# Optimization experiments

Hardware: AMD Instinct MI355X
Metric: run time of the kernel (lower is better)

Reference implementation:

```python
import jax, jax.numpy as jnp
import numpy as np

N, K, H, W = 2048, 8, 128, 128
G = 50              # glimpse size (50x50 from tem_rnn input 50*50)
ENC = 100           # glimpse encoder output (relation_rnn input arithmetic)
HID = 256
D_REL = ENC + (3 + 50) * 2 + HID          # 462
D_TEM = G * G + (3 + 50) * 2 + HID        # 2862


def _lin(k, out_d, in_d, scale=0.02):
    k1, k2 = jax.random.split(k)
    return (jax.random.normal(k1, (out_d, in_d), jnp.float32) * scale,
            jax.random.normal(k2, (out_d,), jnp.float32) * scale)


def _lstm_params(k, in_d, hid):
    k1, k2, k3, k4 = jax.random.split(k, 4)
    s = 0.02
    return (jax.random.normal(k1, (4 * hid, in_d), jnp.float32) * s,
            jax.random.normal(k2, (4 * hid, hid), jnp.float32) * s,
            jax.random.normal(k3, (4 * hid,), jnp.float32) * s,
            jax.random.normal(k4, (4 * hid,), jnp.float32) * s)


def lstm_cell(x, h, c, Wih, Whh, bih, bhh):
    g = x @ Wih.T + h @ Whh.T + (bih + bhh)
    i, f, gg, o = jnp.split(g, 4, axis=-1)
    i, f, o = jax.nn.sigmoid(i), jax.nn.sigmoid(f), jax.nn.sigmoid(o)
    c2 = f * c + i * jnp.tanh(gg)
    return o * jnp.tanh(c2), c2


def _bilinear_one(im, py, px):
    # im [H,W]; py,px [G,G] pixel coords; zeros padding like torch grid_sample
    x0 = jnp.floor(px); y0 = jnp.floor(py)
    wx1 = px - x0; wy1 = py - y0
    x0i = x0.astype(jnp.int32); y0i = y0.astype(jnp.int32)

    def gather(yi, xi):
        valid = (yi >= 0) & (yi < H) & (xi >= 0) & (xi < W)
        v = im[jnp.clip(yi, 0, H - 1), jnp.clip(xi, 0, W - 1)]
        return jnp.where(valid, v, 0.0)

    return ((1 - wy1) * (1 - wx1) * gather(y0i, x0i)
            + (1 - wy1) * wx1 * gather(y0i, x0i + 1)
            + wy1 * (1 - wx1) * gather(y0i + 1, x0i)
            + wy1 * wx1 * gather(y0i + 1, x0i + 1))


def stn_glimpse(z_where, img):
    # z_where [n,3] = (scale, tx, ty); theta = [[s,0,tx],[0,s,ty]] (attentive_stn_encode)
    s, tx, ty = z_where[:, 0], z_where[:, 1], z_where[:, 2]
    lin = jnp.linspace(-1.0, 1.0, G)
    gy, gx = jnp.meshgrid(lin, lin, indexing='ij')           # [G,G]
    px = (s[:, None, None] * gx + tx[:, None, None] + 1.0) * 0.5 * (W - 1)
    py = (s[:, None, None] * gy + ty[:, None, None] + 1.0) * 0.5 * (H - 1)
    out = jax.vmap(_bilinear_one)(img, py, px)               # [n,G,G]
    return out.reshape(out.shape[0], G * G)


def setup_inputs() -> dict:
    key = jax.random.key(0)
    ks = jax.random.split(key, 16)
    inp = {
        'img': jax.random.uniform(ks[0], (N, H, W), jnp.float32),
        'z_what_last': jax.random.normal(ks[1], (N, K, 50), jnp.float32),
        'z_where_last': jax.random.normal(ks[2], (N, K, 3), jnp.float32) * 0.3,
        'z_pres_last': jnp.ones((N, K, 1), jnp.float32),
        'hidden_last': jax.random.normal(ks[3], (N, K, HID), jnp.float32),
    }
    inp['W_loca'], inp['b_loca'] = _lin(ks[4], 3, HID)
    inp['Wg'], inp['bg'] = _lin(ks[5], ENC, G * G)
    (inp['Wih_rel'], inp['Whh_rel'], inp['bih_rel'], inp['bhh_rel']) = _lstm_params(ks[6], D_REL, HID)
    (inp['Wih_tem'], inp['Whh_tem'], inp['bih_tem'], inp['bhh_tem']) = _lstm_params(ks[7], D_TEM, HID)
    inp['Wm_wh'], inp['bm_wh'] = _lin(ks[8], 3, HID + 3)
    inp['Ws_wh'], inp['bs_wh'] = _lin(ks[9], 3, HID + 3)
    inp['Wm_wt'], inp['bm_wt'] = _lin(ks[10], 50, 50 + HID + HID)
    inp['Ws_wt'], inp['bs_wt'] = _lin(ks[11], 50, 50 + HID + HID)
    inp['Wm_pr'], inp['bm_pr'] = _lin(ks[12], 1, 50 + 3 + HID + HID)
    inp['Ws_pr'], inp['bs_pr'] = _lin(ks[13], 1, 50 + 3 + HID + HID)
    return inp


def reference(img, z_what_last, z_where_last, z_pres_last, hidden_last,
              W_loca, b_loca, Wg, bg,
              Wih_rel, Whh_rel, bih_rel, bhh_rel,
              Wih_tem, Whh_tem, bih_tem, bhh_tem,
              Wm_wh, bm_wh, Ws_wh, bs_wh,
              Wm_wt, bm_wt, Ws_wt, bs_wt,
              Wm_pr, bm_pr, Ws_pr, bs_pr):
    n = img.shape[0]

    def step(carry, xs):
        h_r, c_r, pzw, pzwhat = carry
        zwl, zwhatl, zpl, hl = xs   # [n,3],[n,50],[n,1],[n,256]
        # prop_loca: relu(linear(hidden)) + z_where_last
        zwb = jax.nn.relu(hl @ W_loca.T + b_loca) + zwl
        # STN glimpse + encode (bias pass)
        enc = jax.nn.relu(stn_glimpse(zwb, img) @ Wg.T + bg)        # [n,100]
        rin = jnp.concatenate([enc, zwl, pzw, zwhatl, pzwhat, hl], -1)  # [n,462]
        h_r2, c_r2 = lstm_cell(rin, h_r, c_r, Wih_rel, Whh_rel, bih_rel, bhh_rel)
        # z_where: latent predictor mean (eval mode)
        zw = jnp.concatenate([zwl, h_r2], -1) @ Wm_wh.T + bm_wh      # [n,3]
        # second STN glimpse with sampled where
        g2 = stn_glimpse(zw, img)                                    # [n,2500]
        tin = jnp.concatenate([g2, zw, pzw, zwhatl, pzwhat, hl], -1) # [n,2862]
        h_t, c_t = lstm_cell(tin, h_r2, c_r2, Wih_tem, Whh_tem, bih_tem, bhh_tem)
        # z_what mean
        zwhat = jnp.concatenate([zwhatl, h_r2, h_t], -1) @ Wm_wt.T + bm_wt  # [n,50]
        # z_pres: deterministic expectation of Bernoulli(mean*std) * previous pres
        zp_cal = jnp.concatenate([zwhat, zw, h_r2, h_t], -1)
        p = jax.nn.sigmoid(zp_cal @ Wm_pr.T + bm_pr) * jax.nn.sigmoid(zp_cal @ Ws_pr.T + bs_pr)
        zp = p * zpl                                                 # [n,1]
        return (h_r2, c_r2, zw, zwhat), (zwhat, zw, zp, h_t)

    carry0 = (jnp.zeros((n, HID), img.dtype), jnp.zeros((n, HID), img.dtype),
              jnp.zeros((n, 3), img.dtype), jnp.zeros((n, 50), img.dtype))
    xs = (jnp.swapaxes(z_where_last, 0, 1), jnp.swapaxes(z_what_last, 0, 1),
          jnp.swapaxes(z_pres_last, 0, 1), jnp.swapaxes(hidden_last, 0, 1))
    _, (zwhat_s, zw_s, zp_s, ht_s) = jax.lax.scan(step, carry0, xs)
    z_what = jnp.swapaxes(zwhat_s, 0, 1)   # [n,K,50]
    z_where = jnp.swapaxes(zw_s, 0, 1)     # [n,K,3]
    z_pres = jnp.swapaxes(zp_s, 0, 1)      # [n,K,1]
    h_temp = jnp.swapaxes(ht_s, 0, 1)      # [n,K,256]
    return z_what, z_where, z_pres, h_temp
```

## Files before the change

kernel.cpp:

```cpp
#include <hip/hip_runtime.h>
#include <hip/hip_bf16.h>
#include <math.h>

typedef __attribute__((ext_vector_type(8))) short bf16x8;
typedef __attribute__((ext_vector_type(4))) float f32x4;
using bf16 = __hip_bfloat16;

constexpr int NN   = 2048;
constexpr int KO   = 8;
constexpr int IH   = 128, IW = 128;
constexpr int GS   = 50;
constexpr int GG2  = GS*GS;
constexpr int HIDD = 256;
constexpr int RIN_LD = 768;
constexpr int TIN_LD = 3136;
constexpr int G1_LD  = 2560;

__device__ __forceinline__ float sigm(float x) { return 1.f/(1.f+expf(-x)); }

template<int OUT_BF16, int RELU>
__global__ __launch_bounds__(256, 2) void mfma_gemm(
    const bf16* __restrict__ A, int lda, int Kd,
    const bf16* __restrict__ Wt, int ldw, int M,
    const float* __restrict__ b1, const float* __restrict__ b2,
    void* __restrict__ Cout, int ldc)
{
    __shared__ bf16x8 As16[512];
    __shared__ bf16x8 Bs16[512];
    const int tid  = threadIdx.x;
    const int n0   = blockIdx.y*64;
    const int m0   = blockIdx.x*64;
    const int wave = tid>>6, lane = tid&63;
    const int wy   = wave>>1, wx = wave&1;

    const int row = tid>>2, part = tid&3;
    const bf16* Ap = A + (size_t)(n0+row)*lda + part*8;
    const int   wm = m0 + row;
    const bool  wok = wm < M;
    const bf16* Wp = Wt + (size_t)(wok ? wm : 0)*ldw + part*8;
    const int dst0 = ((row>>4)*2+0)*64 + part*16 + (row&15);
    const int dst1 = dst0 + 64;

    f32x4 acc[2][2] = {};
    const bf16x8 z8 = {};
    bf16x8 pa0 = *(const bf16x8*)Ap;
    bf16x8 pa1 = *(const bf16x8*)(Ap + 32);
    bf16x8 pw0 = *(const bf16x8*)Wp;
    bf16x8 pw1 = *(const bf16x8*)(Wp + 32);

    for (int k0 = 0; k0 < Kd; k0 += 64) {
        __syncthreads();
        As16[dst0] = pa0;
        As16[dst1] = pa1;
        Bs16[dst0] = wok ? pw0 : z8;
        Bs16[dst1] = wok ? pw1 : z8;
        __syncthreads();
        if (k0 + 64 < Kd) {
            pa0 = *(const bf16x8*)(Ap + k0 + 64);
            pa1 = *(const bf16x8*)(Ap + k0 + 96);
            pw0 = *(const bf16x8*)(Wp + k0 + 64);
            pw1 = *(const bf16x8*)(Wp + k0 + 96);
        }
        bf16x8 av[2][2], bv[2][2];
        #pragma unroll
        for (int i=0;i<2;i++)
            #pragma unroll
            for (int h=0;h<2;h++) av[i][h] = As16[((wy*2+i)*2+h)*64 + lane];
        #pragma unroll
        for (int j=0;j<2;j++)
            #pragma unroll
            for (int h=0;h<2;h++) bv[j][h] = Bs16[((wx*2+j)*2+h)*64 + lane];
        #pragma unroll
        for (int h=0;h<2;h++)
            #pragma unroll
            for (int i=0;i<2;i++)
                #pragma unroll
                for (int j=0;j<2;j++)
                    acc[i][j] = __builtin_amdgcn_mfma_f32_16x16x32_bf16(av[i][h], bv[j][h], acc[i][j], 0, 0, 0);
    }

    const int q = lane>>4, r = lane&15;
    #pragma unroll
    for (int j=0;j<2;j++) {
        int col = m0 + wx*32 + j*16 + r;
        if (col < M) {
            float bias = 0.f;
            if (b1) bias += b1[col];
            if (b2) bias += b2[col];
            #pragma unroll
            for (int i=0;i<2;i++) {
                #pragma unroll
                for (int reg=0;reg<4;reg++) {
                    float v = acc[i][j][reg] + bias;
                    if (RELU) v = fmaxf(v, 0.f);
                    size_t idx = (size_t)(n0 + wy*32 + i*16 + q*4 + reg)*ldc + col;
                    if (OUT_BF16) ((bf16*)Cout)[idx] = __float2bfloat16(v);
                    else          ((float*)Cout)[idx] = v;
                }
            }
        }
    }
}

__device__ __forceinline__ void glimpse_points(const float* __restrict__ im,
                                               float s, float tx, float ty,
                                               bf16* __restrict__ drow) {
    const float GXS = 2.0f/49.0f;
    const float txp = tx + 1.0f, typ = ty + 1.0f;
    for (int p2 = threadIdx.x; p2 < 1250; p2 += 256) {
        int i = p2 / 25;
        int j = (p2 - i*25) * 2;
        float gy  = fmaf((float)i, GXS, -1.0f);
        float py  = fmaf(s, gy, typ) * 63.5f;
        float y0f = floorf(py); float fy = py - y0f; int y0 = (int)y0f;
        float wy0 = ((unsigned)y0     < 128u) ? (1.f - fy) : 0.f;
        float wy1 = ((unsigned)(y0+1) < 128u) ? fy         : 0.f;
        const float* r0 = im + min(max(y0,  0),127)*IW;
        const float* r1 = im + min(max(y0+1,0),127)*IW;
        float gxa = fmaf((float)j, GXS, -1.0f);
        float pxa = fmaf(s, gxa, txp) * 63.5f;
        float xa0f = floorf(pxa); float fa = pxa - xa0f; int xa0 = (int)xa0f;
        float wa0 = ((unsigned)xa0     < 128u) ? (1.f - fa) : 0.f;
        float wa1 = ((unsigned)(xa0+1) < 128u) ? fa         : 0.f;
        int xa0c = min(max(xa0,  0),127), xa1c = min(max(xa0+1,0),127);
        float gxb = fmaf((float)(j+1), GXS, -1.0f);
        float pxb = fmaf(s, gxb, txp) * 63.5f;
        float xb0f = floorf(pxb); float fb = pxb - xb0f; int xb0 = (int)xb0f;
        float wb0 = ((unsigned)xb0     < 128u) ? (1.f - fb) : 0.f;
        float wb1 = ((unsigned)(xb0+1) < 128u) ? fb         : 0.f;
        int xb0c = min(max(xb0,  0),127), xb1c = min(max(xb0+1,0),127);

        float va = fmaf(wy1, fmaf(wa0, r1[xa0c], wa1*r1[xa1c]),
                   wy0 *     fmaf(wa0, r0[xa0c], wa1*r0[xa1c]));
        float vb = fmaf(wy1, fmaf(wb0, r1[xb0c], wb1*r1[xb1c]),
                   wy0 *     fmaf(wb0, r0[xb0c], wb1*r0[xb1c]));

        bf16 b0 = __float2bfloat16(va), b1 = __float2bfloat16(vb);
        unsigned short u0, u1;
        __builtin_memcpy(&u0, &b0, 2); __builtin_memcpy(&u1, &b1, 2);
        *(unsigned int*)(drow + i*GS + j) = (unsigned)u0 | ((unsigned)u1 << 16);
    }
}

__global__ __launch_bounds__(256) void glimpse_batch(const float* __restrict__ img,
                                                     const float* __restrict__ z,
                                                     bf16* __restrict__ dst, int ldd) {
    int b = blockIdx.x;
    const float* im = img + (size_t)(b & (NN-1))*IH*IW;
    glimpse_points(im, z[b*3+0], z[b*3+1], z[b*3+2], dst + (size_t)b*ldd);
}

__global__ __launch_bounds__(256) void glimpse2_fused(const float* __restrict__ img,
                                                      const float* __restrict__ zw_cur,
                                                      const float* __restrict__ zw_prev,
                                                      const float* __restrict__ zwhat_prev,
                                                      const float* __restrict__ z_what_last,
                                                      const float* __restrict__ hidden_last,
                                                      bf16* __restrict__ tin, int k) {
    int n = blockIdx.x;
    const float* im = img + (size_t)n*IH*IW;
    float s  = zw_cur[n*3+0];
    float tx = zw_cur[n*3+1];
    float ty = zw_cur[n*3+2];
    bf16* trow = tin + (size_t)n*TIN_LD;
    glimpse_points(im, s, tx, ty, trow);
    for (int c = threadIdx.x; c < 362; c += 256) {
        float v;
        if      (c <   3) v = (c==0) ? s : ((c==1) ? tx : ty);
        else if (c <   6) v = zw_prev[n*3 + c-3];
        else if (c <  56) v = z_what_last[((size_t)n*KO + k)*50 + c-6];
        else if (c < 106) v = zwhat_prev[n*50 + c-56];
        else              v = hidden_last[((size_t)n*KO + k)*HIDD + c-106];
        trow[2500 + c] = __float2bfloat16(v);
    }
}

__global__ void zero_f32(float* __restrict__ p, int n) {
    int i = blockIdx.x*blockDim.x + threadIdx.x;
    if (i < n) p[i] = 0.f;
}

__global__ void repack_w(const float* __restrict__ s1, int K1,
                         const float* __restrict__ s2, int K2,
                         bf16* __restrict__ dst, int ldd, int M) {
    int gid = blockIdx.x*blockDim.x + threadIdx.x;
    if (gid >= M*ldd) return;
    int m = gid / ldd, c = gid - m*ldd;
    float v = 0.f;
    if (c < K1)           v = s1[(size_t)m*K1 + c];
    else if (c < K1+K2)   v = s2[(size_t)m*K2 + (c-K1)];
    dst[gid] = __float2bfloat16(v);
}

__global__ void zwb_all_kernel(const float* __restrict__ hidden_last,
                               const float* __restrict__ z_where_last,
                               const float* __restrict__ Wl, const float* __restrict__ bl,
                               float* __restrict__ zwb_all) {
    int gid = blockIdx.x*blockDim.x + threadIdx.x;
    if (gid >= KO*NN*3) return;
    int j = gid % 3; int rn = gid/3; int n = rn & (NN-1); int s = rn >> 11;
    const float* hl = hidden_last + ((size_t)n*KO + s)*HIDD;
    const float* w  = Wl + j*HIDD;
    float acc = bl[j];
    for (int i=0;i<HIDD;i++) acc = fmaf(hl[i], w[i], acc);
    zwb_all[gid] = fmaxf(acc, 0.f) + z_where_last[((size_t)n*KO + s)*3 + j];
}

__global__ void fill_rin_static(bf16* __restrict__ rin,
                                const float* __restrict__ z_where_last,
                                const float* __restrict__ z_what_last,
                                const float* __restrict__ hidden_last,
                                int base, int CH) {
    int gid = blockIdx.x*blockDim.x + threadIdx.x;
    if (gid >= CH*NN*309) return;
    int c = gid % 309; int rn = gid/309; int n = rn & (NN-1); int sl = rn >> 11;
    int k = base + sl;
    float v; int col;
    if (c < 3)       { col = 100 + c;      v = z_where_last[((size_t)n*KO + k)*3 + c]; }
    else if (c < 53) { col = 106 + (c-3);  v = z_what_last[((size_t)n*KO + k)*50 + (c-3)]; }
    else             { col = 206 + (c-53); v = hidden_last[((size_t)n*KO + k)*HIDD + (c-53)]; }
    rin[(size_t)rn*RIN_LD + col] = __float2bfloat16(v);
}

__global__ void zero_rin_carry(bf16* __restrict__ rin0) {
    int gid = blockIdx.x*blockDim.x + threadIdx.x;
    if (gid >= NN*309) return;
    int c = gid % 309, n = gid/309;
    int col = (c < 3) ? 103+c : ((c < 53) ? 156+(c-3) : 462+(c-53));
    rin0[(size_t)n*RIN_LD + col] = __float2bfloat16(0.f);
}

__global__ __launch_bounds__(256) void rel_fused(
    const float* __restrict__ gates, float* __restrict__ h_r, float* __restrict__ c_r,
    const float* __restrict__ z_where_last,
    const float* __restrict__ Wm_wh, const float* __restrict__ bm_wh,
    float* __restrict__ zw_cur, float* __restrict__ out_zwhere,
    bf16* __restrict__ rin_next, bf16* __restrict__ tin, int k)
{
    __shared__ float hs[256];
    int n = blockIdx.x, j = threadIdx.x;
    const float* g = gates + (size_t)n*1024;
    float ig = sigm(g[j]);
    float fg = sigm(g[256+j]);
    float gg = tanhf(g[512+j]);
    float og = sigm(g[768+j]);
    int cidx = n*256 + j;
    float c2 = fg*c_r[cidx] + ig*gg;
    float hv = og*tanhf(c2);
    c_r[cidx] = c2;
    h_r[cidx] = hv;
    hs[j] = hv;
    bf16 hb = __float2bfloat16(hv);
    rin_next[(size_t)n*RIN_LD + 462 + j] = hb;
    tin[(size_t)n*TIN_LD + 2862 + j]     = hb;
    __syncthreads();
    int w = j >> 6, lane = j & 63;
    if (w < 3) {
        const float* wt = Wm_wh + w*259;
        float s = 0.f;
        for (int i = lane; i < 256; i += 64) s = fmaf(hs[i], wt[3+i], s);
        #pragma unroll
        for (int off = 32; off; off >>= 1) s += __shfl_down(s, off);
        if (lane == 0) {
            const float* zwl = z_where_last + ((size_t)n*KO + k)*3;
            float acc = bm_wh[w] + s;
            for (int i = 0; i < 3; i++) acc = fmaf(zwl[i], wt[i], acc);
            zw_cur[n*3+w] = acc;
            out_zwhere[((size_t)n*KO + k)*3 + w] = acc;
            rin_next[(size_t)n*RIN_LD + 103 + w] = __float2bfloat16(acc);
        }
    }
}

__global__ __launch_bounds__(256) void tem_fused(
    const float* __restrict__ gates, const float* __restrict__ c_r, const float* __restrict__ h_r,
    const float* __restrict__ z_what_last,
    const float* __restrict__ Wm_wt, const float* __restrict__ bm_wt,
    const float* __restrict__ Wm_pr, const float* __restrict__ bm_pr,
    const float* __restrict__ Ws_pr, const float* __restrict__ bs_pr,
    const float* __restrict__ zw_cur, const float* __restrict__ z_pres_last,
    float* __restrict__ zwhat_cur, float* __restrict__ out_zwhat,
    float* __restrict__ out_htemp, float* __restrict__ out_zpres,
    bf16* __restrict__ rin_next, int k)
{
    __shared__ float L[615];
    int n = blockIdx.x, j = threadIdx.x;
    const float* g = gates + (size_t)n*1024;
    float ig = sigm(g[j]);
    float fg = sigm(g[256+j]);
    float gg = tanhf(g[512+j]);
    float og = sigm(g[768+j]);
    float c2 = fg*c_r[n*256+j] + ig*gg;
    float hv = og*tanhf(c2);
    out_htemp[((size_t)n*KO + k)*HIDD + j] = hv;
    L[309+j] = hv;
    L[53+j]  = h_r[n*256+j];
    if (j < 50)      L[j]  = z_what_last[((size_t)n*KO + k)*50 + j];
    else if (j < 53) L[j]  = zw_cur[n*3 + (j-50)];
    __syncthreads();
    if (j < 200) {
        int m = j >> 2, part = j & 3;
        const float* wt = Wm_wt + m*562;
        float s = 0.f;
        for (int i = part; i < 562; i += 4) {
            float v = (i < 50) ? L[i] : L[i+3];
            s = fmaf(v, wt[i], s);
        }
        s += __shfl_down(s, 2);
        s += __shfl_down(s, 1);
        if (part == 0) {
            float acc = s + bm_wt[m];
            zwhat_cur[n*50+m] = acc;
            out_zwhat[((size_t)n*KO + k)*50 + m] = acc;
            rin_next[(size_t)n*RIN_LD + 156 + m] = __float2bfloat16(acc);
            L[565+m] = acc;
        }
    }
    __syncthreads();
    if (j < 64) {
        float s1 = 0.f, s2 = 0.f;
        for (int i = j; i < 565; i += 64) {
            float v = (i < 50) ? L[565+i] : L[i];
            s1 = fmaf(v, Wm_pr[i], s1);
            s2 = fmaf(v, Ws_pr[i], s2);
        }
        #pragma unroll
        for (int off = 32; off; off >>= 1) { s1 += __shfl_down(s1,off); s2 += __shfl_down(s2,off); }
        if (j == 0) {
            float p = sigm(s1 + bm_pr[0]) * sigm(s2 + bs_pr[0]);
            out_zpres[(size_t)n*KO + k] = p * z_pres_last[(size_t)n*KO + k];
        }
    }
}

extern "C" void kernel_launch(void* const* d_in, const int* in_sizes, int n_in,
                              void* d_out, int out_size, void* d_ws, size_t ws_size,
                              hipStream_t stream) {
    (void)in_sizes; (void)n_in; (void)out_size;
    const float* img          = (const float*)d_in[0];
    const float* z_what_last  = (const float*)d_in[1];
    const float* z_where_last = (const float*)d_in[2];
    const float* z_pres_last  = (const float*)d_in[3];
    const float* hidden_last  = (const float*)d_in[4];
    const float* W_loca = (const float*)d_in[5];
    const float* b_loca = (const float*)d_in[6];
    const float* Wg     = (const float*)d_in[7];
    const float* bg     = (const float*)d_in[8];
    const float* Wih_rel = (const float*)d_in[9];
    const float* Whh_rel = (const float*)d_in[10];
    const float* bih_rel = (const float*)d_in[11];
    const float* bhh_rel = (const float*)d_in[12];
    const float* Wih_tem = (const float*)d_in[13];
    const float* Whh_tem = (const float*)d_in[14];
    const float* bih_tem = (const float*)d_in[15];
    const float* bhh_tem = (const float*)d_in[16];
    const float* Wm_wh = (const float*)d_in[17];
    const float* bm_wh = (const float*)d_in[18];
    const float* Wm_wt = (const float*)d_in[21];
    const float* bm_wt = (const float*)d_in[22];
    const float* Wm_pr = (const float*)d_in[25];
    const float* bm_pr = (const float*)d_in[26];
    const float* Ws_pr = (const float*)d_in[27];
    const float* bs_pr = (const float*)d_in[28];

    char* base_p = (char*)d_ws;
    size_t off = 0;
    auto carve = [&](size_t bytes) -> char* {
        char* r = base_p + off;
        off += (bytes + 255) & ~(size_t)255;
        return r;
    };
    bf16*  tin      = (bf16*) carve((size_t)NN*TIN_LD*2);
    float* gates    = (float*)carve((size_t)NN*1024*4);
    bf16*  W_tem    = (bf16*) carve((size_t)1024*TIN_LD*2);
    bf16*  W_rel    = (bf16*) carve((size_t)1024*RIN_LD*2);
    bf16*  Wg_bf    = (bf16*) carve((size_t)100*G1_LD*2);
    float* zwb_all  = (float*)carve((size_t)KO*NN*3*4);
    float* h_r      = (float*)carve((size_t)NN*HIDD*4);
    float* c_r      = (float*)carve((size_t)NN*HIDD*4);
    float* zw1      = (float*)carve((size_t)NN*3*4);
    float* zwhat1   = (float*)carve((size_t)NN*50*4);
    float* zw0      = (float*)carve((size_t)NN*3*4);
    float* zwhat0   = (float*)carve((size_t)NN*50*4);
    size_t fixed_bytes = off;

    int CH = 1;
    for (int cand : {8, 4, 2}) {
        size_t need = fixed_bytes
                    + (((size_t)cand*NN*G1_LD*2 + 255) & ~(size_t)255)
                    + (((size_t)cand*NN*RIN_LD*2 + 255) & ~(size_t)255);
        if (need <= ws_size) { CH = cand; break; }
    }
    bf16* g1 = nullptr; int g1ld;
    bf16* rin;
    if (CH > 1) {
        g1   = (bf16*)carve((size_t)CH*NN*G1_LD*2);
        rin  = (bf16*)carve((size_t)CH*NN*RIN_LD*2);
        g1ld = G1_LD;
    } else {
        rin  = (bf16*)carve((size_t)NN*RIN_LD*2);
        g1   = tin;
        g1ld = TIN_LD;
    }

    float* out        = (float*)d_out;
    float* out_zwhat  = out;
    float* out_zwhere = out + (size_t)NN*KO*50;
    float* out_zpres  = out_zwhere + (size_t)NN*KO*3;
    float* out_htemp  = out_zpres + (size_t)NN*KO;

    {
        int nz = NN*(HIDD + 3 + 50);
        zero_f32<<<(nz+255)/256, 256, 0, stream>>>(c_r, nz);
    }
    zero_rin_carry<<<(NN*309+255)/256, 256, 0, stream>>>(rin);
    repack_w<<<((1024*RIN_LD)+255)/256, 256, 0, stream>>>(Wih_rel, 462, Whh_rel, 256, W_rel, RIN_LD, 1024);
    repack_w<<<((1024*TIN_LD)+255)/256, 256, 0, stream>>>(Wih_tem, 2862, Whh_tem, 256, W_tem, TIN_LD, 1024);
    repack_w<<<((100*G1_LD)+255)/256, 256, 0, stream>>>(Wg, 2500, nullptr, 0, Wg_bf, G1_LD, 100);
    zwb_all_kernel<<<(KO*NN*3+255)/256, 256, 0, stream>>>(hidden_last, z_where_last, W_loca, b_loca, zwb_all);

    for (int cbase = 0; cbase < KO; cbase += CH) {
        fill_rin_static<<<(CH*NN*309+255)/256, 256, 0, stream>>>(rin, z_where_last, z_what_last, hidden_last, cbase, CH);
        glimpse_batch<<<CH*NN, 256, 0, stream>>>(img, zwb_all + (size_t)cbase*NN*3, g1, g1ld);
        mfma_gemm<1,1><<<dim3(2, CH*32), 256, 0, stream>>>(g1, g1ld, G1_LD, Wg_bf, G1_LD, 100, bg, nullptr, rin, RIN_LD);

        for (int s = 0; s < CH; ++s) {
            int k = cbase + s;
            bf16* rin_k  = rin + (size_t)s*NN*RIN_LD;
            bf16* rin_nx = rin + (size_t)((s+1)%CH)*NN*RIN_LD;
            float* zw_cur     = (k & 1) ? zw1 : zw0;
            float* zw_prev    = (k & 1) ? zw0 : zw1;
            float* zwhat_cur  = (k & 1) ? zwhat1 : zwhat0;
            float* zwhat_prev = (k & 1) ? zwhat0 : zwhat1;

            mfma_gemm<0,0><<<dim3(16, 32), 256, 0, stream>>>(rin_k, RIN_LD, RIN_LD, W_rel, RIN_LD, 1024, bih_rel, bhh_rel, gates, 1024);
            rel_fused<<<NN, 256, 0, stream>>>(gates, h_r, c_r, z_where_last, Wm_wh, bm_wh, zw_cur, out_zwhere, rin_nx, tin, k);
            glimpse2_fused<<<NN, 256, 0, stream>>>(img, zw_cur, zw_prev, zwhat_prev, z_what_last, hidden_last, tin, k);
            mfma_gemm<0,0><<<dim3(16, 32), 256, 0, stream>>>(tin, TIN_LD, TIN_LD, W_tem, TIN_LD, 1024, bih_tem, bhh_tem, gates, 1024);
            tem_fused<<<NN, 256, 0, stream>>>(gates, c_r, h_r, z_what_last, Wm_wt, bm_wt, Wm_pr, bm_pr, Ws_pr, bs_pr,
                                              zw_cur, z_pres_last, zwhat_cur, out_zwhat, out_htemp, out_zpres, rin_nx, k);
        }
    }
}
```

Baseline: 1.348 ms.

## Remap GEMM blocks per XCD, stage glimpse rows in LDS, warp-reduce zwb

The GEMM launch becomes 1D, and block indices are remapped so that blocks sharing an A row-tile land on the same XCD, which should improve L2 reuse across the chiplets. The first-stage glimpse kernel copies only the image rows covered by the glimpse into shared memory (up to 64 rows) and does the bilinear gathers from LDS. It falls back to global reads when the glimpse spans more rows. The zwb projection now uses one wavefront per row with vector loads and a shuffle reduction instead of a serial per-output loop. The risks are the extra LDS footprint, which lowers occupancy for the glimpse kernel, and an added __syncthreads.

```diff
diff --git a/kernel.cpp b/kernel.cpp
--- a/kernel.cpp
+++ b/kernel.cpp
@@ -10,11 +10,11 @@
 constexpr int KO   = 8;
 constexpr int IH   = 128, IW = 128;
 constexpr int GS   = 50;
-constexpr int GG2  = GS*GS;
 constexpr int HIDD = 256;
 constexpr int RIN_LD = 768;
 constexpr int TIN_LD = 3136;
 constexpr int G1_LD  = 2560;
+constexpr int GROWS  = 64;
 
 __device__ __forceinline__ float sigm(float x) { return 1.f/(1.f+expf(-x)); }
 
@@ -23,13 +23,16 @@
     const bf16* __restrict__ A, int lda, int Kd,
     const bf16* __restrict__ Wt, int ldw, int M,
     const float* __restrict__ b1, const float* __restrict__ b2,
-    void* __restrict__ Cout, int ldc)
+    void* __restrict__ Cout, int ldc, int nxb)
 {
     __shared__ bf16x8 As16[512];
     __shared__ bf16x8 Bs16[512];
+    const int b    = blockIdx.x;
+    const int xcd  = b & 7;
+    const int t    = b >> 3;
+    const int n0   = (xcd + 8*(t / nxb))*64;
+    const int m0   = (t % nxb)*64;
     const int tid  = threadIdx.x;
-    const int n0   = blockIdx.y*64;
-    const int m0   = blockIdx.x*64;
     const int wave = tid>>6, lane = tid&63;
     const int wy   = wave>>1, wx = wave&1;
 
@@ -102,29 +105,28 @@
     }
 }
 
-__device__ __forceinline__ void glimpse_points(const float* __restrict__ im,
-                                               float s, float tx, float ty,
-                                               bf16* __restrict__ drow) {
+__device__ __forceinline__ void glimpse_points_global(const float* __restrict__ im,
+                                                      float s, float tx, float ty,
+                                                      bf16* __restrict__ drow) {
     const float GXS = 2.0f/49.0f;
     const float txp = tx + 1.0f, typ = ty + 1.0f;
     for (int p2 = threadIdx.x; p2 < 1250; p2 += 256) {
-        int i = p2 / 25;
-        int j = (p2 - i*25) * 2;
+        int i = p2 / 25, j = (p2 - i*25)*2;
         float gy  = fmaf((float)i, GXS, -1.0f);
-        float py  = fmaf(s, gy, typ) * 63.5f;
+        float py  = fmaf(s, gy, typ)*63.5f;
         float y0f = floorf(py); float fy = py - y0f; int y0 = (int)y0f;
         float wy0 = ((unsigned)y0     < 128u) ? (1.f - fy) : 0.f;
         float wy1 = ((unsigned)(y0+1) < 128u) ? fy         : 0.f;
         const float* r0 = im + min(max(y0,  0),127)*IW;
         const float* r1 = im + min(max(y0+1,0),127)*IW;
         float gxa = fmaf((float)j, GXS, -1.0f);
-        float pxa = fmaf(s, gxa, txp) * 63.5f;
+        float pxa = fmaf(s, gxa, txp)*63.5f;
         float xa0f = floorf(pxa); float fa = pxa - xa0f; int xa0 = (int)xa0f;
         float wa0 = ((unsigned)xa0     < 128u) ? (1.f - fa) : 0.f;
         float wa1 = ((unsigned)(xa0+1) < 128u) ? fa         : 0.f;
         int xa0c = min(max(xa0,  0),127), xa1c = min(max(xa0+1,0),127);
         float gxb = fmaf((float)(j+1), GXS, -1.0f);
-        float pxb = fmaf(s, gxb, txp) * 63.5f;
+        float pxb = fmaf(s, gxb, txp)*63.5f;
         float xb0f = floorf(pxb); float fb = pxb - xb0f; int xb0 = (int)xb0f;
         float wb0 = ((unsigned)xb0     < 128u) ? (1.f - fb) : 0.f;
         float wb1 = ((unsigned)(xb0+1) < 128u) ? fb         : 0.f;
@@ -145,9 +147,63 @@
 __global__ __launch_bounds__(256) void glimpse_batch(const float* __restrict__ img,
                                                      const float* __restrict__ z,
                                                      bf16* __restrict__ dst, int ldd) {
+    __shared__ float rows[GROWS*IW];
     int b = blockIdx.x;
     const float* im = img + (size_t)(b & (NN-1))*IH*IW;
-    glimpse_points(im, z[b*3+0], z[b*3+1], z[b*3+2], dst + (size_t)b*ldd);
+    float s  = z[b*3+0];
+    float tx = z[b*3+1];
+    float ty = z[b*3+2];
+    bf16* drow = dst + (size_t)b*ldd;
+
+    const float GXS = 2.0f/49.0f;
+    const float txp = tx + 1.0f, typ = ty + 1.0f;
+    float pyA = fmaf(s, -1.f, typ)*63.5f;
+    float pyB = fmaf(s,  1.f, typ)*63.5f;
+    int ylo = (int)floorf(fminf(pyA, pyB));
+    int yhi = (int)floorf(fmaxf(pyA, pyB)) + 1;
+    ylo = min(max(ylo, 0), 127);
+    yhi = min(max(yhi, 0), 127);
+    int nrows = yhi - ylo + 1;
+
+    if (nrows <= GROWS) {
+        const float4* src = (const float4*)(im + ylo*IW);
+        float4* d4 = (float4*)rows;
+        int tot = nrows*(IW/4);
+        for (int t = threadIdx.x; t < tot; t += 256) d4[t] = src[t];
+        __syncthreads();
+        for (int p2 = threadIdx.x; p2 < 1250; p2 += 256) {
+            int i = p2 / 25, j = (p2 - i*25)*2;
+            float gy  = fmaf((float)i, GXS, -1.0f);
+            float py  = fmaf(s, gy, typ)*63.5f;
+            float y0f = floorf(py); float fy = py - y0f; int y0 = (int)y0f;
+            float wy0 = ((unsigned)y0     < 128u) ? (1.f - fy) : 0.f;
+            float wy1 = ((unsigned)(y0+1) < 128u) ? fy         : 0.f;
+            const float* r0 = rows + min(max(y0-ylo,   0), nrows-1)*IW;
+            const float* r1 = rows + min(max(y0+1-ylo, 0), nrows-1)*IW;
+            float gxa = fmaf((float)j, GXS, -1.0f);
+            float pxa = fmaf(s, gxa, txp)*63.5f;
+            float xa0f = floorf(pxa); float fa = pxa - xa0f; int xa0 = (int)xa0f;
+            float wa0 = ((unsigned)xa0     < 128u) ? (1.f - fa) : 0.f;
+            float wa1 = ((unsigned)(xa0+1) < 128u) ? fa         : 0.f;
+            int xa0c = min(max(xa0,  0),127), xa1c = min(max(xa0+1,0),127);
+            float gxb = fmaf((float)(j+1), GXS, -1.0f);
+            float pxb = fmaf(s, gxb, txp)*63.5f;
+            float xb0f = floorf(pxb); float fb = pxb - xb0f; int xb0 = (int)xb0f;
+            float wb0 = ((unsigned)xb0     < 128u) ? (1.f - fb) : 0.f;
+            float wb1 = ((unsigned)(xb0+1) < 128u) ? fb         : 0.f;
+            int xb0c = min(max(xb0,  0),127), xb1c = min(max(xb0+1,0),127);
+            float va = fmaf(wy1, fmaf(wa0, r1[xa0c], wa1*r1[xa1c]),
+                       wy0 *     fmaf(wa0, r0[xa0c], wa1*r0[xa1c]));
+            float vb = fmaf(wy1, fmaf(wb0, r1[xb0c], wb1*r1[xb1c]),
+                       wy0 *     fmaf(wb0, r0[xb0c], wb1*r0[xb1c]));
+            bf16 b0 = __float2bfloat16(va), b1 = __float2bfloat16(vb);
+            unsigned short u0, u1;
+            __builtin_memcpy(&u0, &b0, 2); __builtin_memcpy(&u1, &b1, 2);
+            *(unsigned int*)(drow + i*GS + j) = (unsigned)u0 | ((unsigned)u1 << 16);
+        }
+    } else {
+        glimpse_points_global(im, s, tx, ty, drow);
+    }
 }
 
 __global__ __launch_bounds__(256) void glimpse2_fused(const float* __restrict__ img,
@@ -163,7 +219,7 @@
     float tx = zw_cur[n*3+1];
     float ty = zw_cur[n*3+2];
     bf16* trow = tin + (size_t)n*TIN_LD;
-    glimpse_points(im, s, tx, ty, trow);
+    glimpse_points_global(im, s, tx, ty, trow);
     for (int c = threadIdx.x; c < 362; c += 256) {
         float v;
         if      (c <   3) v = (c==0) ? s : ((c==1) ? tx : ty);
@@ -192,18 +248,37 @@
     dst[gid] = __float2bfloat16(v);
 }
 
-__global__ void zwb_all_kernel(const float* __restrict__ hidden_last,
-                               const float* __restrict__ z_where_last,
-                               const float* __restrict__ Wl, const float* __restrict__ bl,
-                               float* __restrict__ zwb_all) {
-    int gid = blockIdx.x*blockDim.x + threadIdx.x;
-    if (gid >= KO*NN*3) return;
-    int j = gid % 3; int rn = gid/3; int n = rn & (NN-1); int s = rn >> 11;
+__global__ __launch_bounds__(256) void zwb_all_v2(const float* __restrict__ hidden_last,
+                                                  const float* __restrict__ z_where_last,
+                                                  const float* __restrict__ Wl, const float* __restrict__ bl,
+                                                  float* __restrict__ zwb_all) {
+    __shared__ float wls[768];
+    for (int i = threadIdx.x; i < 768; i += 256) wls[i] = Wl[i];
+    __syncthreads();
+    int wv = threadIdx.x>>6, lane = threadIdx.x&63;
+    int row = blockIdx.x*4 + wv;
+    int s = row >> 11, n = row & (NN-1);
     const float* hl = hidden_last + ((size_t)n*KO + s)*HIDD;
-    const float* w  = Wl + j*HIDD;
-    float acc = bl[j];
-    for (int i=0;i<HIDD;i++) acc = fmaf(hl[i], w[i], acc);
-    zwb_all[gid] = fmaxf(acc, 0.f) + z_where_last[((size_t)n*KO + s)*3 + j];
+    float4 h4 = *(const float4*)(hl + lane*4);
+    float s0=0.f, s1=0.f, s2=0.f;
+    #pragma unroll
+    for (int r4=0;r4<4;r4++) {
+        float hv = ((const float*)&h4)[r4];
+        int i = lane*4 + r4;
+        s0 = fmaf(hv, wls[i],     s0);
+        s1 = fmaf(hv, wls[256+i], s1);
+        s2 = fmaf(hv, wls[512+i], s2);
+    }
+    #pragma unroll
+    for (int off=32; off; off>>=1) {
+        s0 += __shfl_down(s0,off); s1 += __shfl_down(s1,off); s2 += __shfl_down(s2,off);
+    }
+    if (lane == 0) {
+        const float* zwl = z_where_last + ((size_t)n*KO + s)*3;
+        zwb_all[row*3+0] = fmaxf(s0+bl[0],0.f) + zwl[0];
+        zwb_all[row*3+1] = fmaxf(s1+bl[1],0.f) + zwl[1];
+        zwb_all[row*3+2] = fmaxf(s2+bl[2],0.f) + zwl[2];
+    }
 }
 
 __global__ void fill_rin_static(bf16* __restrict__ rin,
@@ -417,12 +492,12 @@
     repack_w<<<((1024*RIN_LD)+255)/256, 256, 0, stream>>>(Wih_rel, 462, Whh_rel, 256, W_rel, RIN_LD, 1024);
     repack_w<<<((1024*TIN_LD)+255)/256, 256, 0, stream>>>(Wih_tem, 2862, Whh_tem, 256, W_tem, TIN_LD, 1024);
     repack_w<<<((100*G1_LD)+255)/256, 256, 0, stream>>>(Wg, 2500, nullptr, 0, Wg_bf, G1_LD, 100);
-    zwb_all_kernel<<<(KO*NN*3+255)/256, 256, 0, stream>>>(hidden_last, z_where_last, W_loca, b_loca, zwb_all);
+    zwb_all_v2<<<KO*NN/4, 256, 0, stream>>>(hidden_last, z_where_last, W_loca, b_loca, zwb_all);
 
     for (int cbase = 0; cbase < KO; cbase += CH) {
         fill_rin_static<<<(CH*NN*309+255)/256, 256, 0, stream>>>(rin, z_where_last, z_what_last, hidden_last, cbase, CH);
         glimpse_batch<<<CH*NN, 256, 0, stream>>>(img, zwb_all + (size_t)cbase*NN*3, g1, g1ld);
-        mfma_gemm<1,1><<<dim3(2, CH*32), 256, 0, stream>>>(g1, g1ld, G1_LD, Wg_bf, G1_LD, 100, bg, nullptr, rin, RIN_LD);
+        mfma_gemm<1,1><<<2*CH*32, 256, 0, stream>>>(g1, g1ld, G1_LD, Wg_bf, G1_LD, 100, bg, nullptr, rin, RIN_LD, 2);
 
         for (int s = 0; s < CH; ++s) {
             int k = cbase + s;
@@ -433,10 +508,10 @@
             float* zwhat_cur  = (k & 1) ? zwhat1 : zwhat0;
             float* zwhat_prev = (k & 1) ? zwhat0 : zwhat1;
 
-            mfma_gemm<0,0><<<dim3(16, 32), 256, 0, stream>>>(rin_k, RIN_LD, RIN_LD, W_rel, RIN_LD, 1024, bih_rel, bhh_rel, gates, 1024);
+            mfma_gemm<0,0><<<512, 256, 0, stream>>>(rin_k, RIN_LD, RIN_LD, W_rel, RIN_LD, 1024, bih_rel, bhh_rel, gates, 1024, 16);
             rel_fused<<<NN, 256, 0, stream>>>(gates, h_r, c_r, z_where_last, Wm_wh, bm_wh, zw_cur, out_zwhere, rin_nx, tin, k);
             glimpse2_fused<<<NN, 256, 0, stream>>>(img, zw_cur, zw_prev, zwhat_prev, z_what_last, hidden_last, tin, k);
-            mfma_gemm<0,0><<<dim3(16, 32), 256, 0, stream>>>(tin, TIN_LD, TIN_LD, W_tem, TIN_LD, 1024, bih_tem, bhh_tem, gates, 1024);
+            mfma_gemm<0,0><<<512, 256, 0, stream>>>(tin, TIN_LD, TIN_LD, W_tem, TIN_LD, 1024, bih_tem, bhh_tem, gates, 1024, 16);
             tem_fused<<<NN, 256, 0, stream>>>(gates, c_r, h_r, z_what_last, Wm_wt, bm_wt, Wm_pr, bm_pr, Ws_pr, bs_pr,
                                               zw_cur, z_pres_last, zwhat_cur, out_zwhat, out_htemp, out_zpres, rin_nx, k);
         }
```

After: 1.344 ms. About the same (-0.3%).
